# Performance work log

Hardware: AMD Instinct MI355X
Metric: run time of the kernel (lower is better)

The kernel has to match this reference:

```python
import jax, jax.numpy as jnp
import numpy as np
import math

B, L, D, H = 4, 1024, 1024, 16
HD = D // H  # head dim = 64


def setup_inputs() -> dict:
    key = jax.random.key(0)
    ks = jax.random.split(key, 8)
    s = 1.0 / math.sqrt(D)
    return {
        "Q": jax.random.normal(ks[0], (B, L, D), jnp.float32),
        "K": jax.random.normal(ks[1], (B, L, D), jnp.float32),
        "V": jax.random.normal(ks[2], (B, L, D), jnp.float32),
        "valid_lens": jax.random.randint(ks[3], (B * H * L,), 0, L, jnp.int32),
        "Wq": jax.random.normal(ks[4], (D, D), jnp.float32) * s,
        "Wk": jax.random.normal(ks[5], (D, D), jnp.float32) * s,
        "Wv": jax.random.normal(ks[6], (D, D), jnp.float32) * s,
        "Wo": jax.random.normal(ks[7], (D, D), jnp.float32) * s,
    }


def _split_heads(X):
    # [B, L, D] -> [B*H, L, HD]
    return X.reshape(B, L, H, HD).transpose(0, 2, 1, 3).reshape(B * H, L, HD)


def reference(Q, K, V, valid_lens, Wq, Wk, Wv, Wo):
    q = _split_heads(Q @ Wq.T)
    k = _split_heads(K @ Wk.T)
    v = _split_heads(V @ Wv.T)
    # scaled dot-product scores: [B*H, Lq, Lk]
    scores = jnp.einsum("bqd,bkd->bqk", q, k) / math.sqrt(HD)
    # original flattens scores to [B*H*Lq, Lk] and masks with a
    # [len(valid_lens), Lq] mask (Lq == Lk here) of -1e6, then softmax
    mask = jnp.arange(L)[None, :] < valid_lens[:, None]  # [B*H*L, L]
    flat = jnp.where(mask, scores.reshape(-1, L), jnp.float32(-1e6))
    attn = jax.nn.softmax(flat, axis=-1).reshape(B * H, L, L)
    out = jnp.einsum("bqk,bkd->bqd", attn, v)  # dropout p=0 is identity
    # merge heads: [B*H, L, HD] -> [B, L, D]
    out = out.reshape(B, H, L, HD).transpose(0, 2, 1, 3).reshape(B, L, D)
    return out @ Wo.T
```

## Files before the change

kernel.cpp:

```cpp
#include <hip/hip_runtime.h>
#include <hip/hip_bf16.h>

typedef short v8s __attribute__((ext_vector_type(8)));
typedef unsigned short v8u __attribute__((ext_vector_type(8)));
typedef float v4f __attribute__((ext_vector_type(4)));
typedef unsigned short u16;

#define LL 1024
#define DD 1024

static __device__ __forceinline__ u16 f2b(float x) {
  __hip_bfloat16 h = __float2bfloat16(x);
  return __builtin_bit_cast(u16, h);
}

static __device__ __forceinline__ void gload_lds16(const u16* g, u16* l) {
  __builtin_amdgcn_global_load_lds((const __attribute__((address_space(1))) void*)g,
                                   (__attribute__((address_space(3))) void*)l, 16, 0, 0);
}

__global__ __launch_bounds__(256) void cvt3(const float* __restrict__ p0,
                                            const float* __restrict__ p1,
                                            const float* __restrict__ p2,
                                            u16* __restrict__ out, int n8, long ostride) {
  const float* src = blockIdx.y == 0 ? p0 : (blockIdx.y == 1 ? p1 : p2);
  u16* dst = out + (long)blockIdx.y * ostride;
  int i = blockIdx.x * 256 + threadIdx.x;
  if (i >= n8) return;
  const float4* p = (const float4*)src + (long)i * 2;
  float4 a = p[0], b = p[1];
  v8u r;
  r[0] = f2b(a.x); r[1] = f2b(a.y); r[2] = f2b(a.z); r[3] = f2b(a.w);
  r[4] = f2b(b.x); r[5] = f2b(b.y); r[6] = f2b(b.z); r[7] = f2b(b.w);
  *((v8u*)dst + i) = r;
}

__global__ __launch_bounds__(256) void sortperm(const int* __restrict__ valid,
                                                u16* __restrict__ perm) {
  __shared__ int hist[1024];
  __shared__ int wsum[4];
  const int bh = blockIdx.x;
  const int tid = threadIdx.x;
  const int* v = valid + bh * 1024;
  for (int i = tid; i < 1024; i += 256) hist[i] = 0;
  __syncthreads();
  for (int i = tid; i < 1024; i += 256) {
    int k = v[i];
    k = (k == 0) ? 1023 : (k - 1);
    atomicAdd(&hist[k], 1);
  }
  __syncthreads();
  const int base = tid * 4;
  int h0 = hist[base], h1 = hist[base + 1], h2 = hist[base + 2], h3 = hist[base + 3];
  int local = h0 + h1 + h2 + h3;
  const int lane = tid & 63, w = tid >> 6;
  int scan = local;
#pragma unroll
  for (int d = 1; d < 64; d <<= 1) {
    int t = __shfl_up(scan, d);
    if (lane >= d) scan += t;
  }
  if (lane == 63) wsum[w] = scan;
  __syncthreads();
  int woff = 0;
  for (int i = 0; i < w; ++i) woff += wsum[i];
  int excl = woff + scan - local;
  hist[base] = excl;
  hist[base + 1] = excl + h0;
  hist[base + 2] = excl + h0 + h1;
  hist[base + 3] = excl + h0 + h1 + h2;
  __syncthreads();
  for (int i = tid; i < 1024; i += 256) {
    int k = v[i];
    k = (k == 0) ? 1023 : (k - 1);
    int pos = atomicAdd(&hist[k], 1);
    perm[bh * 1024 + pos] = (u16)i;
  }
}

template <typename OUTT>
__global__ __launch_bounds__(256) void gemm_bt(const u16* __restrict__ A,
                                               const u16* __restrict__ Bw,
                                               OUTT* __restrict__ C,
                                               long za, long zb, long zc) {
  __shared__ u16 As[128 * 64];
  __shared__ u16 Bs[128 * 64];
  A += (long)blockIdx.z * za;
  Bw += (long)blockIdx.z * zb;
  C += (long)blockIdx.z * zc;
  const int tid = threadIdx.x;
  const int lane = tid & 63;
  const int l15 = lane & 15, lg = lane >> 4;
  const int wid = tid >> 6;
  const int wm = wid >> 1, wn = wid & 1;
  const long mbase = (long)blockIdx.y * 128;
  const long nbase = (long)blockIdx.x * 128;

  const u16* ap = A + (mbase + (tid >> 3)) * 1024 + (tid & 7) * 8;
  const u16* bp = Bw + (nbase + (tid >> 3)) * 1024 + (tid & 7) * 8;

  v4f acc[4][4] = {};

  for (int kt = 0; kt < 16; ++kt) {
    __syncthreads();
#pragma unroll
    for (int j = 0; j < 4; ++j) {
      gload_lds16(ap + kt * 64 + j * 32 * 1024, &As[(tid + 256 * j) * 8]);
      gload_lds16(bp + kt * 64 + j * 32 * 1024, &Bs[(tid + 256 * j) * 8]);
    }
    __syncthreads();
#pragma unroll
    for (int kk = 0; kk < 2; ++kk) {
      v8s a[4], b[4];
#pragma unroll
      for (int i = 0; i < 4; ++i)
        a[i] = *(const v8s*)&As[(wm * 64 + i * 16 + l15) * 64 + kk * 32 + lg * 8];
#pragma unroll
      for (int i = 0; i < 4; ++i)
        b[i] = *(const v8s*)&Bs[(wn * 64 + i * 16 + l15) * 64 + kk * 32 + lg * 8];
#pragma unroll
      for (int mi = 0; mi < 4; ++mi)
#pragma unroll
        for (int nj = 0; nj < 4; ++nj)
          acc[mi][nj] = __builtin_amdgcn_mfma_f32_16x16x32_bf16(a[mi], b[nj], acc[mi][nj], 0, 0, 0);
    }
  }
#pragma unroll
  for (int mi = 0; mi < 4; ++mi) {
#pragma unroll
    for (int r = 0; r < 4; ++r) {
      long row = mbase + wm * 64 + mi * 16 + lg * 4 + r;
#pragma unroll
      for (int nj = 0; nj < 4; ++nj) {
        long col = nbase + wn * 64 + nj * 16 + l15;
        if constexpr (__is_same(OUTT, float))
          C[row * 1024 + col] = acc[mi][nj][r];
        else
          C[row * 1024 + col] = f2b(acc[mi][nj][r]);
      }
    }
  }
}

__global__ __launch_bounds__(256) void attn_kern(const u16* __restrict__ qb,
                                                 const u16* __restrict__ kb,
                                                 const u16* __restrict__ vb,
                                                 const int* __restrict__ valid,
                                                 const u16* __restrict__ perm,
                                                 u16* __restrict__ ob) {
  __shared__ u16 Ks[64 * 72];
  __shared__ u16 Vt[64 * 72];
  __shared__ u16 Ps[4][16 * 72];

  const int tid = threadIdx.x;
  const int lane = tid & 63;
  const int wid = tid >> 6;
  const int l15 = lane & 15, lg = lane >> 4;
  const int bh = blockIdx.y;
  const int b = bh >> 4, h = bh & 15;
  const long headoff = ((long)b * LL) * DD + h * 64;
  const int gq = 15 - (int)blockIdx.x;
  const u16* pblk = perm + bh * 1024 + gq * 64;
  const u16* pp = pblk + wid * 16;

  const int qrowA = pp[l15];
  v8s qf[2];
#pragma unroll
  for (int ks = 0; ks < 2; ++ks)
    qf[ks] = *(const v8s*)(qb + headoff + (long)qrowA * DD + ks * 32 + lg * 8);

  int orow[4], vraw[4];
#pragma unroll
  for (int r = 0; r < 4; ++r) {
    int rr = pp[lg * 4 + r];
    orow[r] = rr;
    vraw[r] = valid[bh * LL + rr];
  }
  const int lastv = valid[bh * LL + pblk[63]];
  const int ntiles = ((lastv == 0 ? LL : lastv) + 63) >> 6;

  float mrow[4], lrow[4];
  v4f oacc[4] = {};
#pragma unroll
  for (int r = 0; r < 4; ++r) { mrow[r] = -1e30f; lrow[r] = 0.0f; }

  const int kk = tid & 63;
  const int qtr = tid >> 6;
  const long stagebase = headoff + (long)kk * DD + qtr * 16;

  v8s rk0 = *(const v8s*)(kb + stagebase);
  v8s rk1 = *(const v8s*)(kb + stagebase + 8);
  v8s rv0 = *(const v8s*)(vb + stagebase);
  v8s rv1 = *(const v8s*)(vb + stagebase + 8);

  for (int kt = 0; kt < ntiles; ++kt) {
    __builtin_amdgcn_sched_barrier(0);
    __builtin_amdgcn_s_barrier();
    __builtin_amdgcn_sched_barrier(0);

    *(v8s*)&Ks[kk * 72 + qtr * 16] = rk0;
    *(v8s*)&Ks[kk * 72 + qtr * 16 + 8] = rk1;
    {
      v8u u0 = __builtin_bit_cast(v8u, rv0);
      v8u u1 = __builtin_bit_cast(v8u, rv1);
#pragma unroll
      for (int j = 0; j < 8; ++j) Vt[(qtr * 16 + j) * 72 + kk] = u0[j];
#pragma unroll
      for (int j = 0; j < 8; ++j) Vt[(qtr * 16 + 8 + j) * 72 + kk] = u1[j];
    }
    if (kt + 1 < ntiles) {
      const long noff = stagebase + (long)(kt + 1) * 64 * DD;
      rk0 = *(const v8s*)(kb + noff);
      rk1 = *(const v8s*)(kb + noff + 8);
      rv0 = *(const v8s*)(vb + noff);
      rv1 = *(const v8s*)(vb + noff + 8);
    }
    asm volatile("s_waitcnt lgkmcnt(0)" ::: "memory");
    __builtin_amdgcn_sched_barrier(0);
    __builtin_amdgcn_s_barrier();
    __builtin_amdgcn_sched_barrier(0);

    v4f s[4];
    __builtin_amdgcn_s_setprio(1);
#pragma unroll
    for (int t = 0; t < 4; ++t) {
      v4f z = {};
#pragma unroll
      for (int ks = 0; ks < 2; ++ks) {
        v8s kf = *(const v8s*)&Ks[(t * 16 + l15) * 72 + ks * 32 + lg * 8];
        z = __builtin_amdgcn_mfma_f32_16x16x32_bf16(qf[ks], kf, z, 0, 0, 0);
      }
      s[t] = z;
    }
    __builtin_amdgcn_s_setprio(0);

    const float SC = 0.18033688f;
    const int colbase = kt * 64 + l15;
#pragma unroll
    for (int t = 0; t < 4; ++t)
#pragma unroll
      for (int r = 0; r < 4; ++r) {
        float val = s[t][r] * SC;
        s[t][r] = (colbase + t * 16 < vraw[r]) ? val : -1e6f;
      }

    float pm[4];
#pragma unroll
    for (int r = 0; r < 4; ++r)
      pm[r] = fmaxf(fmaxf(s[0][r], s[1][r]), fmaxf(s[2][r], s[3][r]));
#pragma unroll
    for (int d = 1; d < 16; d <<= 1)
#pragma unroll
      for (int r = 0; r < 4; ++r) pm[r] = fmaxf(pm[r], __shfl_xor(pm[r], d));

    bool sk = true;
#pragma unroll
    for (int r = 0; r < 4; ++r) sk = sk && (pm[r] <= mrow[r] + 11.0f);
    if (!__all(sk)) {
#pragma unroll
      for (int r = 0; r < 4; ++r) {
        float mn = fmaxf(mrow[r], pm[r]);
        float sc = __builtin_amdgcn_exp2f(mrow[r] - mn);
        mrow[r] = mn;
        lrow[r] *= sc;
#pragma unroll
        for (int t = 0; t < 4; ++t) oacc[t][r] *= sc;
      }
    }
    float rs[4] = {0.f, 0.f, 0.f, 0.f};
#pragma unroll
    for (int t = 0; t < 4; ++t)
#pragma unroll
      for (int r = 0; r < 4; ++r) {
        float p = __builtin_amdgcn_exp2f(s[t][r] - mrow[r]);
        s[t][r] = p;
        rs[r] += p;
      }
#pragma unroll
    for (int d = 1; d < 16; d <<= 1)
#pragma unroll
      for (int r = 0; r < 4; ++r) rs[r] += __shfl_xor(rs[r], d);
#pragma unroll
    for (int r = 0; r < 4; ++r) lrow[r] += rs[r];

#pragma unroll
    for (int t = 0; t < 4; ++t)
#pragma unroll
      for (int r = 0; r < 4; ++r)
        Ps[wid][(lg * 4 + r) * 72 + t * 16 + l15] = f2b(s[t][r]);

    asm volatile("s_waitcnt lgkmcnt(0)" ::: "memory");
    __builtin_amdgcn_sched_barrier(0);

    __builtin_amdgcn_s_setprio(1);
#pragma unroll
    for (int ks = 0; ks < 2; ++ks) {
      v8s pa = *(const v8s*)&Ps[wid][l15 * 72 + ks * 32 + lg * 8];
#pragma unroll
      for (int t = 0; t < 4; ++t) {
        v8s vf = *(const v8s*)&Vt[(t * 16 + l15) * 72 + ks * 32 + lg * 8];
        oacc[t] = __builtin_amdgcn_mfma_f32_16x16x32_bf16(pa, vf, oacc[t], 0, 0, 0);
      }
    }
    __builtin_amdgcn_s_setprio(0);
  }

#pragma unroll
  for (int r = 0; r < 4; ++r) {
    float inv = 1.0f / lrow[r];
    long rp = headoff + (long)orow[r] * DD;
#pragma unroll
    for (int t = 0; t < 4; ++t)
      ob[rp + t * 16 + l15] = f2b(oacc[t][r] * inv);
  }
}

extern "C" void kernel_launch(void* const* d_in, const int* in_sizes, int n_in,
                              void* d_out, int out_size, void* d_ws, size_t ws_size,
                              hipStream_t stream) {
  const float* Q = (const float*)d_in[0];
  const float* K = (const float*)d_in[1];
  const float* V = (const float*)d_in[2];
  const int* valid = (const int*)d_in[3];
  const float* Wq = (const float*)d_in[4];
  const float* Wk = (const float*)d_in[5];
  const float* Wv = (const float*)d_in[6];
  const float* Wo = (const float*)d_in[7];
  float* out = (float*)d_out;

  u16* ws = (u16*)d_ws;
  const long MK = 4096L * 1024;
  const long NK = 1024L * 1024;
  u16* qkvb = ws;
  u16* wqkv = qkvb + 3 * MK;
  u16* wo = wqkv + 3 * NK;
  u16* proj = wo + NK;
  u16* ob = proj + 3 * MK;
  u16* perm = qkvb;

  cvt3<<<dim3(2048, 3), 256, 0, stream>>>(Q, K, V, qkvb, (int)(MK / 8), MK);
  cvt3<<<dim3(512, 3), 256, 0, stream>>>(Wq, Wk, Wv, wqkv, (int)(NK / 8), NK);
  cvt3<<<dim3(512, 1), 256, 0, stream>>>(Wo, Wo, Wo, wo, (int)(NK / 8), 0);

  gemm_bt<u16><<<dim3(8, 32, 3), 256, 0, stream>>>(qkvb, wqkv, proj, MK, NK, MK);
  sortperm<<<64, 256, 0, stream>>>(valid, perm);
  attn_kern<<<dim3(16, 64), 256, 0, stream>>>(proj, proj + MK, proj + 2 * MK, valid, perm, ob);
  gemm_bt<float><<<dim3(8, 32, 1), 256, 0, stream>>>(ob, wo, out, 0, 0, 0);
}
```

Baseline: 154.8 us.

## Split attention key range into two chunks and merge partials in a new kernel

Each query group's key tiles are split into two halves of up to 8 tiles, each handled by its own block. Every block writes an unnormalized bf16 partial output plus per-row running max and sum to scratch space. A new merge kernel rescales and combines the two partials into the final normalized output. The aim is more parallelism and a shorter tail from the long-valid-length groups, at the cost of an extra launch, extra memory traffic, and bf16 rounding of the partial outputs.

```diff
diff --git a/kernel.cpp b/kernel.cpp
--- a/kernel.cpp
+++ b/kernel.cpp
@@ -12,6 +12,10 @@
 static __device__ __forceinline__ u16 f2b(float x) {
   __hip_bfloat16 h = __float2bfloat16(x);
   return __builtin_bit_cast(u16, h);
+}
+static __device__ __forceinline__ float b2f(u16 u) {
+  unsigned int x = ((unsigned int)u) << 16;
+  return __builtin_bit_cast(float, x);
 }
 
 static __device__ __forceinline__ void gload_lds16(const u16* g, u16* l) {
@@ -147,7 +151,9 @@
                                                  const u16* __restrict__ vb,
                                                  const int* __restrict__ valid,
                                                  const u16* __restrict__ perm,
-                                                 u16* __restrict__ ob) {
+                                                 u16* __restrict__ partO,
+                                                 float* __restrict__ partM,
+                                                 float* __restrict__ partL) {
   __shared__ u16 Ks[64 * 72];
   __shared__ u16 Vt[64 * 72];
   __shared__ u16 Ps[4][16 * 72];
@@ -159,8 +165,18 @@
   const int bh = blockIdx.y;
   const int b = bh >> 4, h = bh & 15;
   const long headoff = ((long)b * LL) * DD + h * 64;
-  const int gq = 15 - (int)blockIdx.x;
+  const int xx = blockIdx.x;
+  const int gq = 15 - (xx >> 1);
+  const int ch = xx & 1;
   const u16* pblk = perm + bh * 1024 + gq * 64;
+
+  const int lastv = valid[bh * LL + pblk[63]];
+  const int ntiles = ((lastv == 0 ? LL : lastv) + 63) >> 6;
+  const int kt0 = ch * 8;
+  const int kt1 = min(ntiles, kt0 + 8);
+  if (kt0 >= kt1) return;
+  const int slot = (bh * 16 + gq) * 2 + ch;
+
   const u16* pp = pblk + wid * 16;
 
   const int qrowA = pp[l15];
@@ -169,15 +185,9 @@
   for (int ks = 0; ks < 2; ++ks)
     qf[ks] = *(const v8s*)(qb + headoff + (long)qrowA * DD + ks * 32 + lg * 8);
 
-  int orow[4], vraw[4];
-#pragma unroll
-  for (int r = 0; r < 4; ++r) {
-    int rr = pp[lg * 4 + r];
-    orow[r] = rr;
-    vraw[r] = valid[bh * LL + rr];
-  }
-  const int lastv = valid[bh * LL + pblk[63]];
-  const int ntiles = ((lastv == 0 ? LL : lastv) + 63) >> 6;
+  int vraw[4];
+#pragma unroll
+  for (int r = 0; r < 4; ++r) vraw[r] = valid[bh * LL + pp[lg * 4 + r]];
 
   float mrow[4], lrow[4];
   v4f oacc[4] = {};
@@ -188,12 +198,12 @@
   const int qtr = tid >> 6;
   const long stagebase = headoff + (long)kk * DD + qtr * 16;
 
-  v8s rk0 = *(const v8s*)(kb + stagebase);
-  v8s rk1 = *(const v8s*)(kb + stagebase + 8);
-  v8s rv0 = *(const v8s*)(vb + stagebase);
-  v8s rv1 = *(const v8s*)(vb + stagebase + 8);
-
-  for (int kt = 0; kt < ntiles; ++kt) {
+  v8s rk0 = *(const v8s*)(kb + stagebase + (long)kt0 * 64 * DD);
+  v8s rk1 = *(const v8s*)(kb + stagebase + (long)kt0 * 64 * DD + 8);
+  v8s rv0 = *(const v8s*)(vb + stagebase + (long)kt0 * 64 * DD);
+  v8s rv1 = *(const v8s*)(vb + stagebase + (long)kt0 * 64 * DD + 8);
+
+  for (int kt = kt0; kt < kt1; ++kt) {
     __builtin_amdgcn_sched_barrier(0);
     __builtin_amdgcn_s_barrier();
     __builtin_amdgcn_sched_barrier(0);
@@ -208,7 +218,7 @@
 #pragma unroll
       for (int j = 0; j < 8; ++j) Vt[(qtr * 16 + 8 + j) * 72 + kk] = u1[j];
     }
-    if (kt + 1 < ntiles) {
+    if (kt + 1 < kt1) {
       const long noff = stagebase + (long)(kt + 1) * 64 * DD;
       rk0 = *(const v8s*)(kb + noff);
       rk1 = *(const v8s*)(kb + noff + 8);
@@ -305,14 +315,70 @@
     __builtin_amdgcn_s_setprio(0);
   }
 
+  u16* po = partO + (long)slot * 4096;
+  float* pmv = partM + slot * 64;
+  float* plv = partL + slot * 64;
 #pragma unroll
   for (int r = 0; r < 4; ++r) {
-    float inv = 1.0f / lrow[r];
-    long rp = headoff + (long)orow[r] * DD;
+    int p = wid * 16 + lg * 4 + r;
+    pmv[p] = mrow[r];
+    plv[p] = lrow[r];
 #pragma unroll
     for (int t = 0; t < 4; ++t)
-      ob[rp + t * 16 + l15] = f2b(oacc[t][r] * inv);
-  }
+      po[p * 64 + t * 16 + l15] = f2b(oacc[t][r]);
+  }
+}
+
+__global__ __launch_bounds__(256) void merge_kern(const int* __restrict__ valid,
+                                                  const u16* __restrict__ perm,
+                                                  const u16* __restrict__ partO,
+                                                  const float* __restrict__ partM,
+                                                  const float* __restrict__ partL,
+                                                  u16* __restrict__ ob) {
+  const int g = blockIdx.x, bh = blockIdx.y;
+  const int b = bh >> 4, h = bh & 15;
+  const u16* pblk = perm + bh * 1024 + g * 64;
+  const int lastv = valid[bh * LL + pblk[63]];
+  const int ntiles = ((lastv == 0 ? LL : lastv) + 63) >> 6;
+  const bool has1 = ntiles > 8;
+  const int p = threadIdx.x >> 2;
+  const int q4 = (threadIdx.x & 3) * 16;
+  const int s0 = (bh * 16 + g) * 2;
+
+  float m0 = partM[s0 * 64 + p], l0 = partL[s0 * 64 + p];
+  float w0 = 1.0f, w1 = 0.0f, L = l0;
+  if (has1) {
+    float m1 = partM[(s0 + 1) * 64 + p], l1 = partL[(s0 + 1) * 64 + p];
+    float M = fmaxf(m0, m1);
+    w0 = __builtin_amdgcn_exp2f(m0 - M);
+    w1 = __builtin_amdgcn_exp2f(m1 - M);
+    L = l0 * w0 + l1 * w1;
+  }
+  const float inv = 1.0f / L;
+
+  const u16* po0 = partO + (long)s0 * 4096 + p * 64 + q4;
+  float acc[16];
+  {
+    v8u x0 = *(const v8u*)po0;
+    v8u x1 = *(const v8u*)(po0 + 8);
+#pragma unroll
+    for (int j = 0; j < 8; ++j) acc[j] = b2f(x0[j]) * w0;
+#pragma unroll
+    for (int j = 0; j < 8; ++j) acc[8 + j] = b2f(x1[j]) * w0;
+  }
+  if (has1) {
+    const u16* po1 = po0 + 4096;
+    v8u y0 = *(const v8u*)po1;
+    v8u y1 = *(const v8u*)(po1 + 8);
+#pragma unroll
+    for (int j = 0; j < 8; ++j) acc[j] += b2f(y0[j]) * w1;
+#pragma unroll
+    for (int j = 0; j < 8; ++j) acc[8 + j] += b2f(y1[j]) * w1;
+  }
+  const int orow = pblk[p];
+  u16* dst = ob + ((long)b * LL + orow) * DD + h * 64 + q4;
+#pragma unroll
+  for (int j = 0; j < 16; ++j) dst[j] = f2b(acc[j] * inv);
 }
 
 extern "C" void kernel_launch(void* const* d_in, const int* in_sizes, int n_in,
@@ -336,7 +402,10 @@
   u16* wo = wqkv + 3 * NK;
   u16* proj = wo + NK;
   u16* ob = proj + 3 * MK;
-  u16* perm = qkvb;
+  u16* perm = wqkv;
+  u16* partO = qkvb;
+  float* partM = (float*)(qkvb + 2048L * 4096);
+  float* partL = partM + 2048L * 64;
 
   cvt3<<<dim3(2048, 3), 256, 0, stream>>>(Q, K, V, qkvb, (int)(MK / 8), MK);
   cvt3<<<dim3(512, 3), 256, 0, stream>>>(Wq, Wk, Wv, wqkv, (int)(NK / 8), NK);
@@ -344,6 +413,8 @@
 
   gemm_bt<u16><<<dim3(8, 32, 3), 256, 0, stream>>>(qkvb, wqkv, proj, MK, NK, MK);
   sortperm<<<64, 256, 0, stream>>>(valid, perm);
-  attn_kern<<<dim3(16, 64), 256, 0, stream>>>(proj, proj + MK, proj + 2 * MK, valid, perm, ob);
+  attn_kern<<<dim3(32, 64), 256, 0, stream>>>(proj, proj + MK, proj + 2 * MK, valid,
+                                              perm, partO, partM, partL);
+  merge_kern<<<dim3(16, 64), 256, 0, stream>>>(valid, perm, partO, partM, partL, ob);
   gemm_bt<float><<<dim3(8, 32, 1), 256, 0, stream>>>(ob, wo, out, 0, 0, 0);
 }
```

Measured after the change: 157.2 us. Within noise of the previous version (+1.5%).
